# Kernel optimization log

Hardware: AMD Instinct MI355X
Metric: run time of the kernel (lower is better)

## Reference

```python
import jax, jax.numpy as jnp
import numpy as np

B, T, N_X, N_U, N_Y, H = 2048, 2048, 4, 2, 1, 64
MIN_X = jnp.array([0.0, 0.0, 0.0, -jnp.inf], dtype=jnp.float32)
MAX_X = jnp.array([10.0, 10.0, 10.0, jnp.inf], dtype=jnp.float32)
MIN_Y = jnp.array([0.0], dtype=jnp.float32)
MAX_Y = jnp.array([10.0], dtype=jnp.float32)


def setup_inputs() -> dict:
    key = jax.random.key(0)
    ks = jax.random.split(key, 6)
    return {
        "x_0": jax.random.uniform(ks[0], (B, N_X), dtype=jnp.float32) * 5.0,
        "u": jax.random.normal(ks[1], (B, T, N_U), dtype=jnp.float32),
        "theta_f": jnp.array([0.1925, 0.2429, 0.1697, 0.0444, 0.1642], dtype=jnp.float32),
        "theta_h": jnp.zeros((1,), dtype=jnp.float32),
        "tau_u": jnp.ones((1,), dtype=jnp.float32),
        "tau_y": jnp.ones((1,), dtype=jnp.float32),
        "W1": jax.random.normal(ks[2], (N_X + N_U + 5, H), dtype=jnp.float32) / np.sqrt(N_X + N_U + 5),
        "b1": jnp.zeros((H,), dtype=jnp.float32),
        "W2": jax.random.normal(ks[3], (H, N_X), dtype=jnp.float32) * 0.05,
        "Wh": jax.random.normal(ks[4], (N_X, N_Y), dtype=jnp.float32),
    }


def reference(x_0, u, theta_f, theta_h, tau_u, tau_y, W1, b1, W2, Wh):
    Bc = x_0.shape[0]
    tf = jnp.broadcast_to(theta_f[None, :], (Bc, theta_f.shape[0]))
    scale = tau_u[0] / tau_y[0]

    def f(x, ut):
        feat = jnp.concatenate([x, ut, tf], axis=-1)  # (B, n_x+n_u+5)
        return jnp.tanh(feat @ W1 + b1) @ W2 * scale  # (B, n_x)

    def h(x):
        return x @ Wh + theta_h  # (B, n_y)

    y0 = h(x_0)  # unclamped initial output, as in the torch loop

    def step(carry, ut):
        x_step, y_step = carry
        dx = f(x_step, ut)
        x_raw = x_step + dx
        y_new = jnp.clip(h(x_raw), MIN_Y, MAX_Y)  # y computed from pre-clamp state
        x_new = jnp.clip(x_raw, MIN_X, MAX_X)
        return (x_new, y_new), (x_step, y_step)

    u_t = jnp.moveaxis(u, 1, 0)  # (T, B, n_u)
    _, (xs, ys) = jax.lax.scan(step, (x_0, y0), u_t)
    x = jnp.moveaxis(xs, 0, 1)  # (B, T, n_x)
    y = jnp.moveaxis(ys, 0, 1)  # (B, T, n_y)
    return (x, y)
```

## Files before the change

kernel.cpp:

```cpp
#include <hip/hip_runtime.h>

#define B_SZ 2048
#define T_SZ 2048

using f32x16 = float __attribute__((ext_vector_type(16)));
using f32x2  = float __attribute__((ext_vector_type(2)));

template<int CTRL>
__device__ __forceinline__ float dppf(float v) {
  int r = __builtin_amdgcn_update_dpp(0, __builtin_bit_cast(int, v), CTRL, 0xf, 0xf, true);
  return __builtin_bit_cast(float, r);
}

__device__ __forceinline__ f32x2 pkfma(f32x2 a, f32x2 b, f32x2 c) {
  return __builtin_elementwise_fma(a, b, c);
}

__global__ __launch_bounds__(256, 1) void sss_kernel(
    const float* __restrict__ x0p, const float* __restrict__ up,
    const float* __restrict__ tfp, const float* __restrict__ thp,
    const float* __restrict__ tup, const float* __restrict__ typ,
    const float* __restrict__ W1p, const float* __restrict__ b1p,
    const float* __restrict__ W2p, const float* __restrict__ Whp,
    float* __restrict__ outp)
{
  const int lane = threadIdx.x & 63;
  const int wv   = __builtin_amdgcn_readfirstlane((int)(threadIdx.x >> 6));
  const int grp  = lane >> 4;
  const int sl   = lane & 15;
  const int k    = lane & 3;
  const int b    = blockIdx.x * 16 + wv * 4 + grp;

  const float K = 2.8853900817779268f;
  f32x2 w1_01[6], w1_23[6];
#pragma unroll
  for (int r = 0; r < 6; ++r) {
    w1_01[r] = f32x2{W1p[r * 64 + sl]      * K, W1p[r * 64 + sl + 16] * K};
    w1_23[r] = f32x2{W1p[r * 64 + sl + 32] * K, W1p[r * 64 + sl + 48] * K};
  }
  float ccs[4];
#pragma unroll
  for (int i = 0; i < 4; ++i) {
    const int u = sl + 16 * i;
    float t = b1p[u];
#pragma unroll
    for (int q = 0; q < 5; ++q) t = fmaf(tfp[q], W1p[(6 + q) * 64 + u], t);
    ccs[i] = t * K;
  }
  const f32x2 cc01 = f32x2{ccs[0], ccs[1]};
  const f32x2 cc23 = f32x2{ccs[2], ccs[3]};

  const float scale = tup[0] / typ[0];
  f32x2 wAB[4], wCD[4];
#pragma unroll
  for (int i = 0; i < 4; ++i) {
    const float4 w2r = ((const float4*)W2p)[sl + 16 * i];
    float col[4] = {w2r.x * scale, w2r.y * scale, w2r.z * scale, w2r.w * scale};
    wAB[i] = f32x2{col[k], col[k ^ 1]};
    wCD[i] = f32x2{col[k ^ 2], col[k ^ 3]};
  }

  const float whl = Whp[k];
  const float th  = thp[0];

  const float lo = (k == 3) ? -__builtin_inff() : 0.0f;
  const float hi = (k == 3) ?  __builtin_inff() : 10.0f;

  float xlane = x0p[b * 4 + k];
  float x0v = dppf<0x00>(xlane);
  float x1v = dppf<0x55>(xlane);
  float x2v = dppf<0xAA>(xlane);
  float x3v = dppf<0xFF>(xlane);

  float p0 = xlane * whl;
  p0 += dppf<0xB1>(p0);
  p0 += dppf<0x4E>(p0);
  float yv = p0 + th;

  unsigned voff, vinc;
  if (sl < 4) {
    voff = (unsigned)(b * (T_SZ * 4) + sl) * 4u;
    vinc = 16u;
  } else {
    voff = (unsigned)((unsigned)B_SZ * T_SZ * 4u + (unsigned)b * T_SZ) * 4u;
    vinc = (sl == 4) ? 4u : 0u;
  }
  const bool doSt = (sl < 5);
  const bool is4  = (sl == 4);
  unsigned vj[8];
  vj[0] = 0u;
#pragma unroll
  for (int j = 1; j < 8; ++j) vj[j] = vj[j - 1] + vinc;
  const unsigned vinc8 = vj[7] + vinc;

  const f32x16* up16 = (const f32x16*)(up + (size_t)b * (T_SZ * 2));
  char* outB = (char*)outp;

  f32x16 uch = up16[0];
  const int NC = T_SZ / 8;

  for (int c = 0; c < NC; ++c) {
    const int g = (c + 1 < NC) ? c + 1 : NC - 1;
    const f32x16 unx = up16[g];
#pragma unroll
    for (int jj = 0; jj < 8; ++jj) {
      const float vdata = is4 ? yv : xlane;
      if (doSt) *(float*)(outB + (voff + vj[jj])) = vdata;

      const float u0 = uch[2 * jj];
      const float u1 = uch[2 * jj + 1];
      const f32x2 u0p = f32x2{u0, u0};
      const f32x2 u1p = f32x2{u1, u1};

      const f32x2 b01 = pkfma(u1p, w1_01[5], pkfma(u0p, w1_01[4], cc01));
      const f32x2 b23 = pkfma(u1p, w1_23[5], pkfma(u0p, w1_23[4], cc23));

      const f32x2 x0s = f32x2{x0v, x0v};
      const f32x2 x1s = f32x2{x1v, x1v};
      const f32x2 x2s = f32x2{x2v, x2v};
      const f32x2 x3s = f32x2{x3v, x3v};
      const f32x2 mA01 = pkfma(x1s, w1_01[1], x0s * w1_01[0]);
      const f32x2 mB01 = pkfma(x3s, w1_01[3], x2s * w1_01[2]);
      const f32x2 a01  = (b01 + mA01) + mB01;
      const f32x2 mA23 = pkfma(x1s, w1_23[1], x0s * w1_23[0]);
      const f32x2 mB23 = pkfma(x3s, w1_23[3], x2s * w1_23[2]);
      const f32x2 a23  = (b23 + mA23) + mB23;

      float h[4];
      {
        const float av[4] = {a01[0], a01[1], a23[0], a23[1]};
#pragma unroll
        for (int i = 0; i < 4; ++i) {
          const float e  = __builtin_amdgcn_exp2f(av[i]);
          const float rr = __builtin_amdgcn_rcpf(e + 1.0f);
          h[i] = fmaf(-2.0f, rr, 1.0f);
        }
      }
      const f32x2 h0s = f32x2{h[0], h[0]};
      const f32x2 h1s = f32x2{h[1], h[1]};
      const f32x2 h2s = f32x2{h[2], h[2]};
      const f32x2 h3s = f32x2{h[3], h[3]};

      f32x2 qAB = h0s * wAB[0];
      qAB = pkfma(h1s, wAB[1], qAB);
      qAB = pkfma(h2s, wAB[2], qAB);
      qAB = pkfma(h3s, wAB[3], qAB);
      f32x2 qCD = h0s * wCD[0];
      qCD = pkfma(h1s, wCD[1], qCD);
      qCD = pkfma(h2s, wCD[2], qCD);
      qCD = pkfma(h3s, wCD[3], qCD);

      float v = (qAB[0] + dppf<0xB1>(qAB[1]))
              + (dppf<0x4E>(qCD[0]) + dppf<0x1B>(qCD[1]));
      v += dppf<0x124>(v);
      v += dppf<0x128>(v);

      const float w = xlane + v;
      xlane = __builtin_amdgcn_fmed3f(w, lo, hi);

      float p = w * whl;
      p += dppf<0xB1>(p);
      p += dppf<0x4E>(p);
      yv = __builtin_amdgcn_fmed3f(p + th, 0.0f, 10.0f);

      x0v = dppf<0x00>(xlane);
      x1v = dppf<0x55>(xlane);
      x2v = dppf<0xAA>(xlane);
      x3v = dppf<0xFF>(xlane);
    }
    voff += vinc8;
    uch = unx;
  }
}

extern "C" void kernel_launch(void* const* d_in, const int* in_sizes, int n_in,
                              void* d_out, int out_size, void* d_ws, size_t ws_size,
                              hipStream_t stream) {
  (void)in_sizes; (void)n_in; (void)out_size; (void)d_ws; (void)ws_size;
  sss_kernel<<<dim3(B_SZ / 16), dim3(256), 0, stream>>>(
      (const float*)d_in[0], (const float*)d_in[1], (const float*)d_in[2],
      (const float*)d_in[3], (const float*)d_in[4], (const float*)d_in[5],
      (const float*)d_in[6], (const float*)d_in[7], (const float*)d_in[8],
      (const float*)d_in[9], (float*)d_out);
}
```

Before: 359.4 us.

## Stage per-step outputs in LDS and flush coalesced float2 stores per chunk

Each step's x and y values are written to a double-buffered LDS staging area instead of straight to global memory. After every 8-step chunk, lanes read them back and issue contiguous float2 stores for x and per-batch 8-float runs for y. This replaces scattered 4-byte stores from only 5 of every 16 lanes with fully used, coalesced writes. In exchange it adds LDS traffic to the serial loop. It also relies on each wavefront reading only its own region with no barrier, which is safe only because the write and read-back are lane-synchronous within the wave.

```diff
diff --git a/kernel.cpp b/kernel.cpp
--- a/kernel.cpp
+++ b/kernel.cpp
@@ -16,6 +16,9 @@
   return __builtin_elementwise_fma(a, b, c);
 }
 
+#define SSTR 264
+#define SBUF (8 * SSTR)
+
 __global__ __launch_bounds__(256, 1) void sss_kernel(
     const float* __restrict__ x0p, const float* __restrict__ up,
     const float* __restrict__ tfp, const float* __restrict__ thp,
@@ -24,12 +27,16 @@
     const float* __restrict__ W2p, const float* __restrict__ Whp,
     float* __restrict__ outp)
 {
-  const int lane = threadIdx.x & 63;
-  const int wv   = __builtin_amdgcn_readfirstlane((int)(threadIdx.x >> 6));
+  __shared__ float stageF[2 * SBUF];
+
+  const int tid  = threadIdx.x;
+  const int lane = tid & 63;
+  const int wv   = __builtin_amdgcn_readfirstlane((int)(tid >> 6));
   const int grp  = lane >> 4;
   const int sl   = lane & 15;
   const int k    = lane & 3;
-  const int b    = blockIdx.x * 16 + wv * 4 + grp;
+  const int b0   = blockIdx.x * 16 + wv * 4;
+  const int b    = b0 + grp;
 
   const float K = 2.8853900817779268f;
   f32x2 w1_01[6], w1_23[6];
@@ -77,35 +84,29 @@
   p0 += dppf<0x4E>(p0);
   float yv = p0 + th;
 
-  unsigned voff, vinc;
-  if (sl < 4) {
-    voff = (unsigned)(b * (T_SZ * 4) + sl) * 4u;
-    vinc = 16u;
-  } else {
-    voff = (unsigned)((unsigned)B_SZ * T_SZ * 4u + (unsigned)b * T_SZ) * 4u;
-    vinc = (sl == 4) ? 4u : 0u;
-  }
-  const bool doSt = (sl < 5);
-  const bool is4  = (sl == 4);
-  unsigned vj[8];
-  vj[0] = 0u;
-#pragma unroll
-  for (int j = 1; j < 8; ++j) vj[j] = vj[j - 1] + vinc;
-  const unsigned vinc8 = vj[7] + vinc;
+  const bool is4 = (sl == 4);
+
+  const int m   = sl;
+  const int xr  = lane >> 4;
+  const int t0  = m >> 1;
+  const int k0  = (2 * m) & 3;
+  const int rdoff = t0 * SSTR + wv * 64 + 16 * xr + k0;
+  const int yoff  = (lane & 7) * SSTR + wv * 64 + 16 * (lane >> 3) + 4;
+  float2* gxp = (float2*)outp + (size_t)(b0 + (lane >> 4)) * (T_SZ * 2) + (lane & 15);
+  float*  gyp = outp + (size_t)B_SZ * T_SZ * 4 + (size_t)(b0 + (lane >> 3)) * T_SZ + (lane & 7);
 
   const f32x16* up16 = (const f32x16*)(up + (size_t)b * (T_SZ * 2));
-  char* outB = (char*)outp;
-
   f32x16 uch = up16[0];
   const int NC = T_SZ / 8;
 
   for (int c = 0; c < NC; ++c) {
     const int g = (c + 1 < NC) ? c + 1 : NC - 1;
     const f32x16 unx = up16[g];
+    float* sw = &stageF[(c & 1) * SBUF + tid];
 #pragma unroll
     for (int jj = 0; jj < 8; ++jj) {
       const float vdata = is4 ? yv : xlane;
-      if (doSt) *(float*)(outB + (voff + vj[jj])) = vdata;
+      sw[jj * SSTR] = vdata;
 
       const float u0 = uch[2 * jj];
       const float u1 = uch[2 * jj + 1];
@@ -168,7 +169,17 @@
       x2v = dppf<0xAA>(xlane);
       x3v = dppf<0xFF>(xlane);
     }
-    voff += vinc8;
+    {
+      const int bb = (c & 1) * SBUF;
+      const float2 xv = *(const float2*)&stageF[bb + rdoff];
+      *gxp = xv;
+      if (lane < 32) {
+        const float yy = stageF[bb + yoff];
+        *gyp = yy;
+      }
+      gxp += 16;
+      gyp += 8;
+    }
     uch = unx;
   }
 }
```

After: 340.9 us, median of 2. 1.05x faster.
